# Performance work log

Hardware: AMD Instinct MI355X
Metric: run time of the kernel (lower is better)

## Reference

```python
import jax, jax.numpy as jnp
import numpy as np

N_NODES = 50000
N_EDGES = 800000
IN_CH = 16
HEADS = 4
OUT_CH = 128
NEG_SLOPE = 0.2  # GATv2Conv default negative_slope


def setup_inputs() -> dict:
    key = jax.random.key(0)
    k1, k2, k3, k4, k5, k6 = jax.random.split(key, 6)
    edge_feat = jax.random.normal(k1, (N_NODES, IN_CH), dtype=jnp.float32)
    edge_index = jax.random.randint(k2, (2, N_EDGES), 0, N_NODES, dtype=jnp.int64)
    s = 1.0 / np.sqrt(IN_CH)
    W_l = jax.random.normal(k3, (IN_CH, HEADS * OUT_CH), dtype=jnp.float32) * s
    W_r = jax.random.normal(k4, (IN_CH, HEADS * OUT_CH), dtype=jnp.float32) * s
    att = jax.random.normal(k5, (HEADS, OUT_CH), dtype=jnp.float32) * (1.0 / np.sqrt(OUT_CH))
    bias = jnp.zeros((HEADS * OUT_CH,), dtype=jnp.float32)
    return {"edge_feat": edge_feat, "edge_index": edge_index,
            "W_l": W_l, "W_r": W_r, "att": att, "bias": bias}


def reference(edge_feat, edge_index, W_l, W_r, att, bias):
    # GATv2Conv forward (eval mode: dropout is identity), concat=True,
    # add_self_loops=True (PyG default).
    N = edge_feat.shape[0]
    loops = jnp.arange(N, dtype=edge_index.dtype)
    ei = jnp.concatenate([edge_index, jnp.stack([loops, loops])], axis=1)
    src, dst = ei[0], ei[1]  # message flows src -> dst

    x_l = (edge_feat @ W_l).reshape(N, HEADS, OUT_CH)  # source transform
    x_r = (edge_feat @ W_r).reshape(N, HEADS, OUT_CH)  # target transform

    # edge-wise GATv2 score: a^T LeakyReLU(x_l[j] + x_r[i])
    e = jax.nn.leaky_relu(x_l[src] + x_r[dst], NEG_SLOPE)  # [E, H, C]
    score = jnp.einsum('ehc,hc->eh', e, att)               # [E, H]

    # segment softmax over incoming edges of each target node
    smax = jax.ops.segment_max(score, dst, num_segments=N)  # [N, H]
    ex = jnp.exp(score - smax[dst])
    denom = jax.ops.segment_sum(ex, dst, num_segments=N)    # [N, H]
    alpha = ex / (denom[dst] + 1e-16)                       # [E, H]

    # scatter-aggregate weighted source features
    out = jax.ops.segment_sum(alpha[:, :, None] * x_l[src], dst, num_segments=N)
    return out.reshape(N, HEADS * OUT_CH) + bias
```

## Files before the change

kernel.cpp:

```cpp
#include <hip/hip_runtime.h>
#include <math.h>

#define N_NODES 50000
#define N_EDGES 800000
#define FDIM 512
#define NEG_SLOPE 0.2f
#define CAP 64

__global__ __launch_bounds__(256) void fill_bucket_kernel(const int* __restrict__ ei,
                                                          int* __restrict__ deg,
                                                          int* __restrict__ bucket) {
    bool is64 = true;
#pragma unroll
    for (int i = 0; i < 16; i++) is64 = is64 && (ei[2 * i + 1] == 0);

    int e = blockIdx.x * 256 + threadIdx.x;
    if (e < N_EDGES) {
        int src = is64 ? ei[2 * e] : ei[e];
        int dst = is64 ? ei[2 * (N_EDGES + e)] : ei[N_EDGES + e];
        int pos = atomicAdd(&deg[dst], 1);
        if (pos < CAP) bucket[dst * CAP + pos] = src;
    }
}

__device__ __forceinline__ unsigned short f2bf(float x) {
    unsigned int u = __float_as_uint(x);
    u = (u + 0x7FFFu + ((u >> 16) & 1u)) >> 16;
    return (unsigned short)u;
}

__global__ __launch_bounds__(256) void gemm_xl_kernel(const float* __restrict__ feat,
                                                      const float* __restrict__ Wl,
                                                      unsigned int* __restrict__ xlb) {
    __shared__ float fsh[64 * 16];
    int t = threadIdx.x;
    int node0 = blockIdx.x * 64;
    int nvalid = min(64, N_NODES - node0);

    float w0[16], w1[16];
#pragma unroll
    for (int k = 0; k < 16; k++) {
        float2 w = ((const float2*)(Wl + k * FDIM))[t];
        w0[k] = w.x; w1[k] = w.y;
    }
    if (t < nvalid * 4) {
        ((float4*)fsh)[t] = ((const float4*)(feat + (size_t)node0 * 16))[t];
    }
    __syncthreads();

    for (int n = 0; n < nvalid; n++) {
        const float4* fq = (const float4*)(fsh + n * 16);
        float4 q0 = fq[0], q1 = fq[1], q2 = fq[2], q3 = fq[3];
        float fr[16] = {q0.x, q0.y, q0.z, q0.w, q1.x, q1.y, q1.z, q1.w,
                        q2.x, q2.y, q2.z, q2.w, q3.x, q3.y, q3.z, q3.w};
        float a0 = 0.f, a1 = 0.f;
#pragma unroll
        for (int k = 0; k < 16; k++) {
            a0 = fmaf(fr[k], w0[k], a0);
            a1 = fmaf(fr[k], w1[k], a1);
        }
        xlb[(size_t)(node0 + n) * 256 + t] =
            (unsigned int)f2bf(a0) | ((unsigned int)f2bf(a1) << 16);
    }
}

#define DPP_ROR_ADD(x, ctrl) \
    ((x) + __int_as_float(__builtin_amdgcn_update_dpp(0, __float_as_int(x), (ctrl), 0xF, 0xF, true)))

__device__ __forceinline__ void unpack8(uint4 u, float* xv) {
    xv[0] = __uint_as_float(u.x << 16); xv[1] = __uint_as_float(u.x & 0xFFFF0000u);
    xv[2] = __uint_as_float(u.y << 16); xv[3] = __uint_as_float(u.y & 0xFFFF0000u);
    xv[4] = __uint_as_float(u.z << 16); xv[5] = __uint_as_float(u.z & 0xFFFF0000u);
    xv[6] = __uint_as_float(u.w << 16); xv[7] = __uint_as_float(u.w & 0xFFFF0000u);
}

__device__ __forceinline__ float partial_score(const float* xv, const float* xr, const float* a) {
    float p = 0.f;
#pragma unroll
    for (int j = 0; j < 8; j++) {
        float s = xv[j] + xr[j];
        float lr = s > 0.f ? s : NEG_SLOPE * s;
        p = fmaf(lr, a[j], p);
    }
    return p;
}

__global__ __launch_bounds__(512) void gat_aggregate_kernel(
        const float* __restrict__ feat, const float* __restrict__ Wr,
        const float* __restrict__ att,  const float* __restrict__ bias,
        const uint4* __restrict__ xlb,  const int* __restrict__ deg,
        const int* __restrict__ bucket, float* __restrict__ out) {
    int t = threadIdx.x;
    int wave = t >> 6, lane = t & 63;
    int node = blockIdx.x * 8 + wave;
    int cbase = lane * 8;

    float f[16];
    {
        const float4* fp = (const float4*)(feat + (size_t)node * 16);
        float4 f0 = fp[0], f1 = fp[1], f2 = fp[2], f3 = fp[3];
        f[0]=f0.x; f[1]=f0.y; f[2]=f0.z; f[3]=f0.w;
        f[4]=f1.x; f[5]=f1.y; f[6]=f1.z; f[7]=f1.w;
        f[8]=f2.x; f[9]=f2.y; f[10]=f2.z; f[11]=f2.w;
        f[12]=f3.x; f[13]=f3.y; f[14]=f3.z; f[15]=f3.w;
    }

    float xr[8];
#pragma unroll
    for (int j = 0; j < 8; j++) xr[j] = 0.f;
#pragma unroll
    for (int k = 0; k < 16; k++) {
        float fk = f[k];
        float4 wa = *(const float4*)(Wr + k * FDIM + cbase);
        float4 wb = *(const float4*)(Wr + k * FDIM + cbase + 4);
        xr[0] = fmaf(fk, wa.x, xr[0]); xr[1] = fmaf(fk, wa.y, xr[1]);
        xr[2] = fmaf(fk, wa.z, xr[2]); xr[3] = fmaf(fk, wa.w, xr[3]);
        xr[4] = fmaf(fk, wb.x, xr[4]); xr[5] = fmaf(fk, wb.y, xr[5]);
        xr[6] = fmaf(fk, wb.z, xr[6]); xr[7] = fmaf(fk, wb.w, xr[7]);
    }

    float a[8];
    {
        float4 a0 = *(const float4*)(att + cbase);
        float4 a1 = *(const float4*)(att + cbase + 4);
        a[0]=a0.x; a[1]=a0.y; a[2]=a0.z; a[3]=a0.w;
        a[4]=a1.x; a[5]=a1.y; a[6]=a1.z; a[7]=a1.w;
    }

    float m = -INFINITY, d = 0.f;
    float acc[8];
#pragma unroll
    for (int j = 0; j < 8; j++) acc[j] = 0.f;

    int dn = min(deg[node], CAP);
    int total = dn + 1;
    const int* brow = bucket + node * CAP;

    for (int k = 0; k < total; k += 4) {
        int r = total - k;
        int4 q = *(const int4*)(brow + k);
        int s0 = (k     < dn) ? q.x : node;
        int s1 = (k + 1 < dn) ? q.y : node;
        int s2 = (k + 2 < dn) ? q.z : node;
        int s3 = (k + 3 < dn) ? q.w : node;

        uint4 u0 = xlb[(size_t)s0 * 64 + lane];
        uint4 u1 = xlb[(size_t)s1 * 64 + lane];
        uint4 u2 = xlb[(size_t)s2 * 64 + lane];
        uint4 u3 = xlb[(size_t)s3 * 64 + lane];

        float x0[8], x1[8], x2[8], x3[8];
        unpack8(u0, x0); unpack8(u1, x1); unpack8(u2, x2); unpack8(u3, x3);

        float p0 = partial_score(x0, xr, a);
        float p1 = partial_score(x1, xr, a);
        float p2 = partial_score(x2, xr, a);
        float p3 = partial_score(x3, xr, a);

        p0 = DPP_ROR_ADD(p0, 0x128); p1 = DPP_ROR_ADD(p1, 0x128);
        p2 = DPP_ROR_ADD(p2, 0x128); p3 = DPP_ROR_ADD(p3, 0x128);
        p0 = DPP_ROR_ADD(p0, 0x124); p1 = DPP_ROR_ADD(p1, 0x124);
        p2 = DPP_ROR_ADD(p2, 0x124); p3 = DPP_ROR_ADD(p3, 0x124);
        p0 = DPP_ROR_ADD(p0, 0x122); p1 = DPP_ROR_ADD(p1, 0x122);
        p2 = DPP_ROR_ADD(p2, 0x122); p3 = DPP_ROR_ADD(p3, 0x122);
        p0 = DPP_ROR_ADD(p0, 0x121); p1 = DPP_ROR_ADD(p1, 0x121);
        p2 = DPP_ROR_ADD(p2, 0x121); p3 = DPP_ROR_ADD(p3, 0x121);

        if (r < 2) p1 = -INFINITY;
        if (r < 3) p2 = -INFINITY;
        if (r < 4) p3 = -INFINITY;

        float nm = fmaxf(fmaxf(fmaxf(m, p0), fmaxf(p1, p2)), p3);
        float sc = __expf(m - nm);
        float w0 = __expf(p0 - nm);
        float w1 = __expf(p1 - nm);
        float w2 = __expf(p2 - nm);
        float w3 = __expf(p3 - nm);
        d = fmaf(d, sc, (w0 + w1) + (w2 + w3));
#pragma unroll
        for (int j = 0; j < 8; j++) {
            float v = acc[j] * sc;
            v = fmaf(w0, x0[j], v);
            v = fmaf(w1, x1[j], v);
            v = fmaf(w2, x2[j], v);
            v = fmaf(w3, x3[j], v);
            acc[j] = v;
        }
        m = nm;
    }

    float inv = 1.f / (d + 1e-16f);
    float4 b0 = *(const float4*)(bias + cbase);
    float4 b1 = *(const float4*)(bias + cbase + 4);
    float bb[8] = {b0.x, b0.y, b0.z, b0.w, b1.x, b1.y, b1.z, b1.w};
    float o[8];
#pragma unroll
    for (int j = 0; j < 8; j++) o[j] = fmaf(acc[j], inv, bb[j]);
    float* op = out + (size_t)node * FDIM + cbase;
    *(float4*)op       = make_float4(o[0], o[1], o[2], o[3]);
    *(float4*)(op + 4) = make_float4(o[4], o[5], o[6], o[7]);
}

extern "C" void kernel_launch(void* const* d_in, const int* in_sizes, int n_in,
                              void* d_out, int out_size, void* d_ws, size_t ws_size,
                              hipStream_t stream) {
    const float* feat = (const float*)d_in[0];
    const int*   ei   = (const int*)d_in[1];
    const float* Wl   = (const float*)d_in[2];
    const float* Wr   = (const float*)d_in[3];
    const float* att  = (const float*)d_in[4];
    const float* bias = (const float*)d_in[5];
    float* out = (float*)d_out;

    char* ws = (char*)d_ws;
    size_t off = 0;
    unsigned int* xlb = (unsigned int*)(ws + off); off += (size_t)N_NODES * 256 * sizeof(unsigned int);
    int* deg    = (int*)(ws + off); off += (size_t)N_NODES * sizeof(int);
    int* bucket = (int*)(ws + off); off += ((size_t)N_NODES * CAP + 16) * sizeof(int);
    (void)ws_size; (void)in_sizes; (void)n_in; (void)out_size;

    hipError_t _e = hipMemsetAsync(deg, 0, (size_t)N_NODES * sizeof(int), stream); (void)_e;
    fill_bucket_kernel<<<(N_EDGES + 255) / 256, 256, 0, stream>>>(ei, deg, bucket);
    gemm_xl_kernel<<<(N_NODES + 63) / 64, 256, 0, stream>>>(feat, Wl, xlb);
    gat_aggregate_kernel<<<N_NODES / 8, 512, 0, stream>>>(
        feat, Wr, att, bias, (const uint4*)xlb, deg, bucket, out);
}
```

Measured before the change: 356.0 us.

## Merge fill and GEMM kernels, double-buffer neighbor gathers in aggregation

The bucket-fill and x_l GEMM kernels are combined into one launch, with block index choosing the role, so the two independent stages run concurrently and one launch is saved. The aggregation loop now double-buffers gathers: the next batch of four neighbor rows is loaded while the current batch is scored and accumulated, which hides gather latency. This raises register pressure from the extra uint4 buffers, which could reduce occupancy.

```diff
diff --git a/kernel.cpp b/kernel.cpp
--- a/kernel.cpp
+++ b/kernel.cpp
@@ -7,21 +7,8 @@
 #define NEG_SLOPE 0.2f
 #define CAP 64
 
-__global__ __launch_bounds__(256) void fill_bucket_kernel(const int* __restrict__ ei,
-                                                          int* __restrict__ deg,
-                                                          int* __restrict__ bucket) {
-    bool is64 = true;
-#pragma unroll
-    for (int i = 0; i < 16; i++) is64 = is64 && (ei[2 * i + 1] == 0);
-
-    int e = blockIdx.x * 256 + threadIdx.x;
-    if (e < N_EDGES) {
-        int src = is64 ? ei[2 * e] : ei[e];
-        int dst = is64 ? ei[2 * (N_EDGES + e)] : ei[N_EDGES + e];
-        int pos = atomicAdd(&deg[dst], 1);
-        if (pos < CAP) bucket[dst * CAP + pos] = src;
-    }
-}
+#define GEMM_BLKS 782
+#define FILL_BLKS 3125
 
 __device__ __forceinline__ unsigned short f2bf(float x) {
     unsigned int u = __float_as_uint(x);
@@ -29,11 +16,28 @@
     return (unsigned short)u;
 }
 
-__global__ __launch_bounds__(256) void gemm_xl_kernel(const float* __restrict__ feat,
+__global__ __launch_bounds__(256) void preproc_kernel(const float* __restrict__ feat,
                                                       const float* __restrict__ Wl,
-                                                      unsigned int* __restrict__ xlb) {
+                                                      unsigned int* __restrict__ xlb,
+                                                      const int* __restrict__ ei,
+                                                      int* __restrict__ deg,
+                                                      int* __restrict__ bucket) {
+    int t = threadIdx.x;
+    if (blockIdx.x >= GEMM_BLKS) {
+        bool is64 = true;
+#pragma unroll
+        for (int i = 0; i < 16; i++) is64 = is64 && (ei[2 * i + 1] == 0);
+        int e = (blockIdx.x - GEMM_BLKS) * 256 + t;
+        if (e < N_EDGES) {
+            int src = is64 ? ei[2 * e] : ei[e];
+            int dst = is64 ? ei[2 * (N_EDGES + e)] : ei[N_EDGES + e];
+            int pos = atomicAdd(&deg[dst], 1);
+            if (pos < CAP) bucket[dst * CAP + pos] = src;
+        }
+        return;
+    }
+
     __shared__ float fsh[64 * 16];
-    int t = threadIdx.x;
     int node0 = blockIdx.x * 64;
     int nvalid = min(64, N_NODES - node0);
 
@@ -83,6 +87,65 @@
         p = fmaf(lr, a[j], p);
     }
     return p;
+}
+
+__device__ __forceinline__ void load_batch(const int* __restrict__ brow, int k, int dn,
+                                           int node, const uint4* __restrict__ xlb,
+                                           int lane, uint4* __restrict__ u) {
+    int4 q = *(const int4*)(brow + k);
+    int s0 = (k     < dn) ? q.x : node;
+    int s1 = (k + 1 < dn) ? q.y : node;
+    int s2 = (k + 2 < dn) ? q.z : node;
+    int s3 = (k + 3 < dn) ? q.w : node;
+    u[0] = xlb[(size_t)s0 * 64 + lane];
+    u[1] = xlb[(size_t)s1 * 64 + lane];
+    u[2] = xlb[(size_t)s2 * 64 + lane];
+    u[3] = xlb[(size_t)s3 * 64 + lane];
+}
+
+__device__ __forceinline__ void process_batch(const uint4* __restrict__ u, int r,
+                                              const float* __restrict__ xr,
+                                              const float* __restrict__ a,
+                                              float* __restrict__ acc,
+                                              float& m, float& d) {
+    float x0[8], x1[8], x2[8], x3[8];
+    unpack8(u[0], x0); unpack8(u[1], x1); unpack8(u[2], x2); unpack8(u[3], x3);
+
+    float p0 = partial_score(x0, xr, a);
+    float p1 = partial_score(x1, xr, a);
+    float p2 = partial_score(x2, xr, a);
+    float p3 = partial_score(x3, xr, a);
+
+    p0 = DPP_ROR_ADD(p0, 0x128); p1 = DPP_ROR_ADD(p1, 0x128);
+    p2 = DPP_ROR_ADD(p2, 0x128); p3 = DPP_ROR_ADD(p3, 0x128);
+    p0 = DPP_ROR_ADD(p0, 0x124); p1 = DPP_ROR_ADD(p1, 0x124);
+    p2 = DPP_ROR_ADD(p2, 0x124); p3 = DPP_ROR_ADD(p3, 0x124);
+    p0 = DPP_ROR_ADD(p0, 0x122); p1 = DPP_ROR_ADD(p1, 0x122);
+    p2 = DPP_ROR_ADD(p2, 0x122); p3 = DPP_ROR_ADD(p3, 0x122);
+    p0 = DPP_ROR_ADD(p0, 0x121); p1 = DPP_ROR_ADD(p1, 0x121);
+    p2 = DPP_ROR_ADD(p2, 0x121); p3 = DPP_ROR_ADD(p3, 0x121);
+
+    if (r < 2) p1 = -INFINITY;
+    if (r < 3) p2 = -INFINITY;
+    if (r < 4) p3 = -INFINITY;
+
+    float nm = fmaxf(fmaxf(fmaxf(m, p0), fmaxf(p1, p2)), p3);
+    float sc = __expf(m - nm);
+    float w0 = __expf(p0 - nm);
+    float w1 = __expf(p1 - nm);
+    float w2 = __expf(p2 - nm);
+    float w3 = __expf(p3 - nm);
+    d = fmaf(d, sc, (w0 + w1) + (w2 + w3));
+#pragma unroll
+    for (int j = 0; j < 8; j++) {
+        float v = acc[j] * sc;
+        v = fmaf(w0, x0[j], v);
+        v = fmaf(w1, x1[j], v);
+        v = fmaf(w2, x2[j], v);
+        v = fmaf(w3, x3[j], v);
+        acc[j] = v;
+    }
+    m = nm;
 }
 
 __global__ __launch_bounds__(512) void gat_aggregate_kernel(
@@ -136,57 +199,21 @@
     int total = dn + 1;
     const int* brow = bucket + node * CAP;
 
-    for (int k = 0; k < total; k += 4) {
-        int r = total - k;
-        int4 q = *(const int4*)(brow + k);
-        int s0 = (k     < dn) ? q.x : node;
-        int s1 = (k + 1 < dn) ? q.y : node;
-        int s2 = (k + 2 < dn) ? q.z : node;
-        int s3 = (k + 3 < dn) ? q.w : node;
-
-        uint4 u0 = xlb[(size_t)s0 * 64 + lane];
-        uint4 u1 = xlb[(size_t)s1 * 64 + lane];
-        uint4 u2 = xlb[(size_t)s2 * 64 + lane];
-        uint4 u3 = xlb[(size_t)s3 * 64 + lane];
-
-        float x0[8], x1[8], x2[8], x3[8];
-        unpack8(u0, x0); unpack8(u1, x1); unpack8(u2, x2); unpack8(u3, x3);
-
-        float p0 = partial_score(x0, xr, a);
-        float p1 = partial_score(x1, xr, a);
-        float p2 = partial_score(x2, xr, a);
-        float p3 = partial_score(x3, xr, a);
-
-        p0 = DPP_ROR_ADD(p0, 0x128); p1 = DPP_ROR_ADD(p1, 0x128);
-        p2 = DPP_ROR_ADD(p2, 0x128); p3 = DPP_ROR_ADD(p3, 0x128);
-        p0 = DPP_ROR_ADD(p0, 0x124); p1 = DPP_ROR_ADD(p1, 0x124);
-        p2 = DPP_ROR_ADD(p2, 0x124); p3 = DPP_ROR_ADD(p3, 0x124);
-        p0 = DPP_ROR_ADD(p0, 0x122); p1 = DPP_ROR_ADD(p1, 0x122);
-        p2 = DPP_ROR_ADD(p2, 0x122); p3 = DPP_ROR_ADD(p3, 0x122);
-        p0 = DPP_ROR_ADD(p0, 0x121); p1 = DPP_ROR_ADD(p1, 0x121);
-        p2 = DPP_ROR_ADD(p2, 0x121); p3 = DPP_ROR_ADD(p3, 0x121);
-
-        if (r < 2) p1 = -INFINITY;
-        if (r < 3) p2 = -INFINITY;
-        if (r < 4) p3 = -INFINITY;
-
-        float nm = fmaxf(fmaxf(fmaxf(m, p0), fmaxf(p1, p2)), p3);
-        float sc = __expf(m - nm);
-        float w0 = __expf(p0 - nm);
-        float w1 = __expf(p1 - nm);
-        float w2 = __expf(p2 - nm);
-        float w3 = __expf(p3 - nm);
-        d = fmaf(d, sc, (w0 + w1) + (w2 + w3));
-#pragma unroll
-        for (int j = 0; j < 8; j++) {
-            float v = acc[j] * sc;
-            v = fmaf(w0, x0[j], v);
-            v = fmaf(w1, x1[j], v);
-            v = fmaf(w2, x2[j], v);
-            v = fmaf(w3, x3[j], v);
-            acc[j] = v;
-        }
-        m = nm;
+    uint4 A[4], B[4];
+    load_batch(brow, 0, dn, node, xlb, lane, A);
+    int k = 0;
+    while (true) {
+        int kB = k + 4;
+        bool hasB = kB < total;
+        if (hasB) load_batch(brow, kB, dn, node, xlb, lane, B);
+        process_batch(A, total - k, xr, a, acc, m, d);
+        if (!hasB) break;
+        int kA = k + 8;
+        bool hasA = kA < total;
+        if (hasA) load_batch(brow, kA, dn, node, xlb, lane, A);
+        process_batch(B, total - kB, xr, a, acc, m, d);
+        if (!hasA) break;
+        k = kA;
     }
 
     float inv = 1.f / (d + 1e-16f);
@@ -220,8 +247,7 @@
     (void)ws_size; (void)in_sizes; (void)n_in; (void)out_size;
 
     hipError_t _e = hipMemsetAsync(deg, 0, (size_t)N_NODES * sizeof(int), stream); (void)_e;
-    fill_bucket_kernel<<<(N_EDGES + 255) / 256, 256, 0, stream>>>(ei, deg, bucket);
-    gemm_xl_kernel<<<(N_NODES + 63) / 64, 256, 0, stream>>>(feat, Wl, xlb);
+    preproc_kernel<<<GEMM_BLKS + FILL_BLKS, 256, 0, stream>>>(feat, Wl, xlb, ei, deg, bucket);
     gat_aggregate_kernel<<<N_NODES / 8, 512, 0, stream>>>(
         feat, Wr, att, bias, (const uint4*)xlb, deg, bucket, out);
 }
```

Result: faster. 342.7 us (-3.7%).
